# Kernel tuning notes

Measured on AMD Instinct MI355X. Metric: run time of the kernel, lower is better.

Reference implementation:

```python
import jax, jax.numpy as jnp
import numpy as np

NUM_HEADS = 16


def setup_inputs() -> dict:
    key = jax.random.key(0)
    k1, k2, k3 = jax.random.split(key, 3)
    B, N, C = 4, 2048, 1024
    x = jax.random.normal(k1, (B, N, C), dtype=jnp.float32)
    w_qkv = jax.random.normal(k2, (C, 3 * C), dtype=jnp.float32) * (C ** -0.5)
    w_proj = jax.random.normal(k3, (C, C), dtype=jnp.float32) * (C ** -0.5)
    b_proj = jnp.zeros((C,), dtype=jnp.float32)
    return {"x": x, "w_qkv": w_qkv, "w_proj": w_proj, "b_proj": b_proj}


def reference(x, w_qkv, w_proj, b_proj):
    B, N, C = x.shape
    H = NUM_HEADS
    hd = C // H
    scale = hd ** -0.5
    # qkv projection (no bias), split into q, k, v per head
    qkv = jnp.einsum('bnc,cd->bnd', x, w_qkv)            # [B, N, 3C]
    qkv = qkv.reshape(B, N, 3, H, hd).transpose(0, 3, 2, 1, 4)  # [B, H, 3, N, hd]
    q, k, v = qkv[:, :, 0], qkv[:, :, 1], qkv[:, :, 2]   # each [B, H, N, hd]
    q = q * scale
    attn = jax.nn.softmax(jnp.einsum('bhnd,bhmd->bhnm', q, k), axis=-1)  # [B, H, N, N]
    out = jnp.einsum('bhnm,bhmd->bhnd', attn, v)         # [B, H, N, hd]
    out = out.transpose(0, 2, 1, 3).reshape(B, N, C)
    return jnp.einsum('bnc,cd->bnd', out, w_proj) + b_proj
```

## Files before the change

### kernel.cpp

```cpp
#include <hip/hip_runtime.h>

typedef short s16x8 __attribute__((ext_vector_type(8)));
typedef float f32x4 __attribute__((ext_vector_type(4)));
typedef float f32x16 __attribute__((ext_vector_type(16)));
typedef unsigned u32x4 __attribute__((ext_vector_type(4)));


__device__ __forceinline__ unsigned short bf16bits(float f) {
  unsigned u = __builtin_bit_cast(unsigned, f);
  unsigned rnd = 0x7FFFu + ((u >> 16) & 1u);
  return (unsigned short)((u + rnd) >> 16);
}

__device__ __forceinline__ unsigned pk_bf16(float lo, float hi) {
  unsigned r;
  asm("v_cvt_pk_bf16_f32 %0, %1, %2" : "=v"(r) : "v"(lo), "v"(hi));
  return r;
}

__device__ __forceinline__ void async16(const void* g, void* l) {
  __builtin_amdgcn_global_load_lds((const __attribute__((address_space(1))) void*)g,
                                   (__attribute__((address_space(3))) void*)l, 16, 0, 0);
}

__device__ __forceinline__ f32x4 mfma16(s16x8 a, s16x8 b, f32x4 c) {
  return __builtin_amdgcn_mfma_f32_16x16x32_bf16(a, b, c, 0, 0, 0);
}

__device__ __forceinline__ f32x16 mfma32(s16x8 a, s16x8 b, f32x16 c) {
  return __builtin_amdgcn_mfma_f32_32x32x16_bf16(a, b, c, 0, 0, 0);
}

__device__ __forceinline__ s16x8 lds_frag(const unsigned short* S, int row, int c8, int U) {
  int unit = row * U + (c8 ^ (row & (U - 1)));
  return *(const s16x8*)(S + unit * 8);
}


__global__ __launch_bounds__(256) void cvt_f32_bf16(const float4* __restrict__ in,
                                                    unsigned short* __restrict__ out, int n4) {
  int i = blockIdx.x * blockDim.x + threadIdx.x;
  int stride = gridDim.x * blockDim.x;
  for (; i < n4; i += stride) {
    float4 v = in[i];
    uint2 o;
    o.x = pk_bf16(v.x, v.y);
    o.y = pk_bf16(v.z, v.w);
    *(uint2*)(out + (size_t)i * 4) = o;
  }
}

__global__ __launch_bounds__(256) void transpose_f32_bf16(const float* __restrict__ in,
                                                          unsigned short* __restrict__ out,
                                                          int R, int C) {
  __shared__ float tile[32][33];
  int c0 = blockIdx.x * 32, r0 = blockIdx.y * 32;
  int tx = threadIdx.x, ty = threadIdx.y;
  #pragma unroll
  for (int i = 0; i < 32; i += 8)
    tile[ty + i][tx] = in[(size_t)(r0 + ty + i) * C + c0 + tx];
  __syncthreads();
  #pragma unroll
  for (int i = 0; i < 32; i += 8)
    out[(size_t)(c0 + ty + i) * R + r0 + tx] = bf16bits(tile[tx][ty + i]);
}

__global__ __launch_bounds__(256) void transpose_v(const unsigned short* __restrict__ V,
                                                   unsigned short* __restrict__ Vt) {
  __shared__ unsigned short sm[64 * 68];
  int bh = blockIdx.y, kt0 = blockIdx.x * 64;
  const unsigned short* v = V + (size_t)bh * 2048 * 64 + (size_t)kt0 * 64;
  unsigned short* vt = Vt + (size_t)bh * 64 * 2048;
  int t = threadIdx.x;
  #pragma unroll
  for (int i = 0; i < 4; ++i) {
    int u = i * 256 + t;
    int f = u * 4;
    int k = f >> 6, d0 = f & 63;
    *(uint2*)&sm[k * 68 + d0] = *(const uint2*)&v[f];
  }
  __syncthreads();
  #pragma unroll
  for (int j = 0; j < 16; ++j) {
    int o = j * 256 + t;
    int d = o >> 6, k = o & 63;
    vt[(size_t)d * 2048 + kt0 + k] = sm[k * 68 + d];
  }
}


template <typename EPI>
__global__ __launch_bounds__(512, 2) void gemm8(const unsigned short* __restrict__ A,
                                                const unsigned short* __restrict__ Bt,
                                                int K, EPI epi) {
  __shared__ __align__(16) unsigned short As[3 * 128 * 64];
  __shared__ __align__(16) unsigned short Bs[3 * 256 * 64];
  const int tid = threadIdx.x, wid = tid >> 6, lane = tid & 63;
  const int quad = lane >> 4, l16 = lane & 15;
  const int bm0 = blockIdx.y * 128, bn0 = blockIdx.x * 256;
  const int wm = (wid & 1) * 64, wn = (wid >> 1) * 64;
  const int NT = K >> 6;
  f32x4 acc[4][4] = {};

  const int srow = tid >> 3;
  const int sc8 = (tid & 7) ^ (srow & 7);
  auto stage = [&](int s, int tk, int k) {
    int col = tk * 64 + sc8 * 8;
    if (k < 2)
      async16(A + (size_t)(bm0 + k * 64 + srow) * K + col,
              (char*)As + s * 16384 + k * 8192 + wid * 1024);
    else
      async16(Bt + (size_t)(bn0 + (k - 2) * 64 + srow) * K + col,
              (char*)Bs + s * 32768 + (k - 2) * 8192 + wid * 1024);
  };

  #pragma unroll
  for (int k = 0; k < 6; ++k) stage(0, 0, k);
  #pragma unroll
  for (int k = 0; k < 6; ++k) stage(1, 1, k);
  asm volatile("s_waitcnt vmcnt(6)" ::: "memory");
  __builtin_amdgcn_s_barrier();
  __builtin_amdgcn_sched_barrier(0);

  int sc = 0;
  for (int t = 0; t < NT; ++t) {
    const unsigned short* as = As + sc * 8192;
    const unsigned short* bs = Bs + sc * 16384;
    const int sp = (sc == 0) ? 2 : sc - 1;
    const bool pf = (t + 2 < NT);

    #pragma unroll
    for (int kk = 0; kk < 2; ++kk) {
      s16x8 a[4], b[4];
      #pragma unroll
      for (int i = 0; i < 4; ++i) a[i] = lds_frag(as, wm + i * 16 + l16, kk * 4 + quad, 8);
      #pragma unroll
      for (int j = 0; j < 4; ++j) b[j] = lds_frag(bs, wn + j * 16 + l16, kk * 4 + quad, 8);
      if (pf) { stage(sp, t + 2, kk * 3 + 0); stage(sp, t + 2, kk * 3 + 1); stage(sp, t + 2, kk * 3 + 2); }
      __builtin_amdgcn_sched_barrier(0);
      __builtin_amdgcn_s_barrier();
      __builtin_amdgcn_s_setprio(1);
      #pragma unroll
      for (int i = 0; i < 4; ++i)
        #pragma unroll
        for (int j = 0; j < 4; ++j)
          acc[i][j] = mfma16(a[i], b[j], acc[i][j]);
      __builtin_amdgcn_s_setprio(0);
      __builtin_amdgcn_sched_barrier(0);
      if (kk == 1) {
        if (pf) asm volatile("s_waitcnt vmcnt(6)" ::: "memory");
        else    asm volatile("s_waitcnt vmcnt(0)" ::: "memory");
      }
      __builtin_amdgcn_s_barrier();
    }
    sc = (sc == 2) ? 0 : sc + 1;
  }

  #pragma unroll
  for (int i = 0; i < 4; ++i)
    #pragma unroll
    for (int j = 0; j < 4; ++j)
      epi.store4(bm0 + wm + i * 16 + quad * 4, bn0 + wn + j * 16 + l16, acc[i][j]);
}

struct QKVEpi {
  unsigned short *Q, *K, *V;
  float qscale;
  __device__ __forceinline__ void store4(int m0, int n, f32x4 v) const {
    int s = m0 >> 10, h = (m0 >> 6) & 15, d = m0 & 63;
    int b = n >> 11, ns = n & 2047;
    unsigned short* dst = (s == 0) ? Q : ((s == 1) ? K : V);
    float sc = (s == 0) ? qscale : 1.f;
    uint2 o;
    o.x = pk_bf16(v[0] * sc, v[1] * sc);
    o.y = pk_bf16(v[2] * sc, v[3] * sc);
    *(uint2*)&dst[(((size_t)b * 16 + h) * 2048 + ns) * 64 + d] = o;
  }
};

struct ProjEpi {
  const float* bias;
  float* out;
  __device__ __forceinline__ void store4(int m0, int n, f32x4 v) const {
    float4 b4 = *(const float4*)&bias[m0];
    float4 o = {v[0] + b4.x, v[1] + b4.y, v[2] + b4.z, v[3] + b4.w};
    *(float4*)&out[(size_t)n * 1024 + m0] = o;
  }
};

__global__ __launch_bounds__(256, 4) void flash_attn(const unsigned short* __restrict__ Q,
                                                     const unsigned short* __restrict__ K,
                                                     const unsigned short* __restrict__ Vt,
                                                     unsigned short* __restrict__ O) {
  __shared__ __align__(16) unsigned short Ks[2][8 * 512];
  __shared__ __align__(16) unsigned short Vs[2][8 * 512];
  const int tid = threadIdx.x, wid = tid >> 6, lane = tid & 63;
  const int l31 = lane & 31, half = lane >> 5;
  const int bid = blockIdx.y * gridDim.x + blockIdx.x;
  const int xcd = bid & 7, idx = bid >> 3;
  const int bh = xcd * 8 + (idx & 7);
  const int qt = idx >> 3;
  const unsigned short* Qg = Q + (size_t)bh * 2048 * 64;
  const unsigned short* Kg = K + (size_t)bh * 2048 * 64;
  const unsigned short* Vg = Vt + (size_t)bh * 64 * 2048;
  const int qrow = qt * 128 + wid * 32 + l31;

  s16x8 qB[4];
  #pragma unroll
  for (int s = 0; s < 4; ++s)
    qB[s] = *(const s16x8*)&Qg[(size_t)qrow * 64 + s * 16 + half * 8];

  const bool isK = wid < 2;
  int sA[4];
  #pragma unroll
  for (int t = 0; t < 4; ++t) {
    int c = (wid & 1) * 4 + t;
    if (isK) sA[t] = ((c >> 2) * 32 + l31) * 64 + ((c & 3) * 2 + half) * 8;
    else     sA[t] = ((c & 1) * 32 + l31) * 2048 + (c >> 1) * 16 + half * 8;
  }

  auto stage = [&](int kt, int buf) {
    const int kb = kt * 64;
    #pragma unroll
    for (int t = 0; t < 4; ++t) {
      int c = (wid & 1) * 4 + t;
      if (isK) async16(Kg + (size_t)kb * 64 + sA[t], (char*)&Ks[buf][0] + c * 1024);
      else     async16(Vg + kb + sA[t],              (char*)&Vs[buf][0] + c * 1024);
    }
  };

  f32x16 oacc[2] = {};
  float l_i = 0.f;
  const f32x16 fz = {};

  stage(0, 0);
  for (int kt = 0; kt < 32; ++kt) {
    const int cur = kt & 1;
    __syncthreads();
    if (kt + 1 < 32) stage(kt + 1, cur ^ 1);
    const unsigned short* ks = &Ks[cur][0];
    const unsigned short* vs = &Vs[cur][0];

    #pragma unroll
    for (int kf = 0; kf < 2; ++kf) {
      f32x16 st;
      __builtin_amdgcn_s_setprio(1);
      {
        s16x8 a = *(const s16x8*)&ks[((kf * 4 + 0) * 64 + lane) * 8];
        st = mfma32(a, qB[0], fz);
      }
      #pragma unroll
      for (int s = 1; s < 4; ++s) {
        s16x8 a = *(const s16x8*)&ks[((kf * 4 + s) * 64 + lane) * 8];
        st = mfma32(a, qB[s], st);
      }
      __builtin_amdgcn_s_setprio(0);
      float a0 = 0.f, a1 = 0.f, a2 = 0.f, a3 = 0.f;
      #pragma unroll
      for (int r = 0; r < 16; r += 4) {
        float p0 = __builtin_amdgcn_exp2f(st[r + 0]);
        float p1 = __builtin_amdgcn_exp2f(st[r + 1]);
        float p2 = __builtin_amdgcn_exp2f(st[r + 2]);
        float p3 = __builtin_amdgcn_exp2f(st[r + 3]);
        st[r + 0] = p0; st[r + 1] = p1; st[r + 2] = p2; st[r + 3] = p3;
        a0 += p0; a1 += p1; a2 += p2; a3 += p3;
      }
      float rs = (a0 + a1) + (a2 + a3);
      rs += __shfl_xor(rs, 32);
      l_i += rs;
      #pragma unroll
      for (int t = 0; t < 2; ++t) {
        int rb = t * 8;
        unsigned pa0 = pk_bf16(st[rb + 0], st[rb + 1]);
        unsigned pa1 = pk_bf16(st[rb + 2], st[rb + 3]);
        unsigned pb0 = pk_bf16(st[rb + 4], st[rb + 5]);
        unsigned pb1 = pk_bf16(st[rb + 6], st[rb + 7]);
        unsigned s0 = half ? pa0 : pb0;
        unsigned s1 = half ? pa1 : pb1;
        unsigned r0 = (unsigned)__shfl_xor((int)s0, 32);
        unsigned r1 = (unsigned)__shfl_xor((int)s1, 32);
        u32x4 bP;
        bP[0] = half ? r0 : pa0;
        bP[1] = half ? r1 : pa1;
        bP[2] = half ? pb0 : r0;
        bP[3] = half ? pb1 : r1;
        __builtin_amdgcn_s_setprio(1);
        #pragma unroll
        for (int f = 0; f < 2; ++f) {
          s16x8 aV = *(const s16x8*)&vs[(((kf * 2 + t) * 2 + f) * 64 + lane) * 8];
          oacc[f] = mfma32(aV, __builtin_bit_cast(s16x8, bP), oacc[f]);
        }
        __builtin_amdgcn_s_setprio(0);
      }
    }
  }

  const int b = bh >> 4, h = bh & 15;
  float inv = 1.f / l_i;
  size_t base = (((size_t)b * 2048 + qrow) * 16 + h) * 64;
  #pragma unroll
  for (int f = 0; f < 2; ++f)
    #pragma unroll
    for (int q = 0; q < 4; ++q) {
      int d0 = f * 32 + q * 8 + half * 4;
      uint2 o;
      o.x = pk_bf16(oacc[f][q * 4 + 0] * inv, oacc[f][q * 4 + 1] * inv);
      o.y = pk_bf16(oacc[f][q * 4 + 2] * inv, oacc[f][q * 4 + 3] * inv);
      *(uint2*)&O[base + d0] = o;
    }
}


extern "C" void kernel_launch(void* const* d_in, const int* in_sizes, int n_in,
                              void* d_out, int out_size, void* d_ws, size_t ws_size,
                              hipStream_t stream) {
  (void)in_sizes; (void)n_in; (void)out_size; (void)ws_size;
  const float* x = (const float*)d_in[0];
  const float* w_qkv = (const float*)d_in[1];
  const float* w_proj = (const float*)d_in[2];
  const float* b_proj = (const float*)d_in[3];
  float* out = (float*)d_out;
  char* ws = (char*)d_ws;
  const size_t MB = 1ull << 20;
  unsigned short* Xb  = (unsigned short*)(ws);
  unsigned short* Wqt = (unsigned short*)(ws + 16 * MB);
  unsigned short* Wpt = (unsigned short*)(ws + 22 * MB);
  unsigned short* Qb  = (unsigned short*)(ws + 24 * MB);
  unsigned short* Kb  = (unsigned short*)(ws + 40 * MB);
  unsigned short* Vb  = (unsigned short*)(ws + 56 * MB);
  unsigned short* Vt  = Xb;
  unsigned short* Ob  = Vb;

  cvt_f32_bf16<<<2048, 256, 0, stream>>>((const float4*)x, Xb, 8388608 / 4);
  transpose_f32_bf16<<<dim3(96, 32), dim3(32, 8), 0, stream>>>(w_qkv, Wqt, 1024, 3072);
  transpose_f32_bf16<<<dim3(32, 32), dim3(32, 8), 0, stream>>>(w_proj, Wpt, 1024, 1024);

  QKVEpi e1{Qb, Kb, Vb, 0.125f * 1.44269504088896340736f};
  gemm8<QKVEpi><<<dim3(32, 24), 512, 0, stream>>>(Wqt, Xb, 1024, e1);

  transpose_v<<<dim3(32, 64), 256, 0, stream>>>(Vb, Vt);
  flash_attn<<<dim3(16, 64), 256, 0, stream>>>(Qb, Kb, Vt, Ob);

  ProjEpi e2{b_proj, out};
  gemm8<ProjEpi><<<dim3(32, 8), 512, 0, stream>>>(Wpt, Ob, 1024, e2);
}
```

Measured before the change: 276.7 us.

## Enlarge GEMM tile to 256x256 with double-buffered LDS pipeline

Replaces the 128x256 GEMM tile, which used a triple-buffered LDS prefetch two steps ahead, with a 256x256 tile that is double-buffered and prefetches one step ahead. Each wave now computes a 128x64 sub-tile in four phases that reuse the loaded B fragments. The aim is more arithmetic per byte loaded and less global traffic. In exchange it doubles accumulator registers, halves the grid (384 and 128 blocks on a 256-CU part), and leaves less prefetch slack, which risks lower occupancy and poorer wave balance, especially for the projection GEMM.

```diff
diff --git a/kernel.cpp b/kernel.cpp
--- a/kernel.cpp
+++ b/kernel.cpp
@@ -90,74 +90,82 @@
 
 
 template <typename EPI>
-__global__ __launch_bounds__(512, 2) void gemm8(const unsigned short* __restrict__ A,
-                                                const unsigned short* __restrict__ Bt,
-                                                int K, EPI epi) {
-  __shared__ __align__(16) unsigned short As[3 * 128 * 64];
-  __shared__ __align__(16) unsigned short Bs[3 * 256 * 64];
+__global__ __launch_bounds__(512, 2) void gemm256(const unsigned short* __restrict__ A,
+                                                  const unsigned short* __restrict__ Bt,
+                                                  int K, EPI epi) {
+  __shared__ __align__(16) unsigned short As[2 * 256 * 64];
+  __shared__ __align__(16) unsigned short Bs[2 * 256 * 64];
   const int tid = threadIdx.x, wid = tid >> 6, lane = tid & 63;
   const int quad = lane >> 4, l16 = lane & 15;
-  const int bm0 = blockIdx.y * 128, bn0 = blockIdx.x * 256;
-  const int wm = (wid & 1) * 64, wn = (wid >> 1) * 64;
+  const int bm0 = blockIdx.y * 256, bn0 = blockIdx.x * 256;
+  const int wm = (wid & 1) * 128, wn = (wid >> 1) * 64;
   const int NT = K >> 6;
-  f32x4 acc[4][4] = {};
+  f32x4 acc[8][4] = {};
 
   const int srow = tid >> 3;
   const int sc8 = (tid & 7) ^ (srow & 7);
-  auto stage = [&](int s, int tk, int k) {
+  auto stage = [&](int s, int tk, int c) {
     int col = tk * 64 + sc8 * 8;
-    if (k < 2)
-      async16(A + (size_t)(bm0 + k * 64 + srow) * K + col,
-              (char*)As + s * 16384 + k * 8192 + wid * 1024);
+    if (c < 4)
+      async16(A + (size_t)(bm0 + c * 64 + srow) * K + col,
+              (char*)As + s * 32768 + c * 8192 + wid * 1024);
     else
-      async16(Bt + (size_t)(bn0 + (k - 2) * 64 + srow) * K + col,
-              (char*)Bs + s * 32768 + (k - 2) * 8192 + wid * 1024);
+      async16(Bt + (size_t)(bn0 + (c - 4) * 64 + srow) * K + col,
+              (char*)Bs + s * 32768 + (c - 4) * 8192 + wid * 1024);
   };
 
   #pragma unroll
-  for (int k = 0; k < 6; ++k) stage(0, 0, k);
-  #pragma unroll
-  for (int k = 0; k < 6; ++k) stage(1, 1, k);
-  asm volatile("s_waitcnt vmcnt(6)" ::: "memory");
+  for (int c = 0; c < 8; ++c) stage(0, 0, c);
+  asm volatile("s_waitcnt vmcnt(0)" ::: "memory");
   __builtin_amdgcn_s_barrier();
   __builtin_amdgcn_sched_barrier(0);
 
-  int sc = 0;
   for (int t = 0; t < NT; ++t) {
-    const unsigned short* as = As + sc * 8192;
-    const unsigned short* bs = Bs + sc * 16384;
-    const int sp = (sc == 0) ? 2 : sc - 1;
-    const bool pf = (t + 2 < NT);
-
-    #pragma unroll
-    for (int kk = 0; kk < 2; ++kk) {
-      s16x8 a[4], b[4];
-      #pragma unroll
-      for (int i = 0; i < 4; ++i) a[i] = lds_frag(as, wm + i * 16 + l16, kk * 4 + quad, 8);
-      #pragma unroll
-      for (int j = 0; j < 4; ++j) b[j] = lds_frag(bs, wn + j * 16 + l16, kk * 4 + quad, 8);
-      if (pf) { stage(sp, t + 2, kk * 3 + 0); stage(sp, t + 2, kk * 3 + 1); stage(sp, t + 2, kk * 3 + 2); }
+    const int s = t & 1;
+    const unsigned short* as = As + s * 16384;
+    const unsigned short* bs = Bs + s * 16384;
+    const bool pf = (t + 1 < NT);
+    s16x8 b[4][2];
+    #pragma unroll
+    for (int p = 0; p < 4; ++p) {
+      if (p == 0) {
+        #pragma unroll
+        for (int j = 0; j < 4; ++j)
+          #pragma unroll
+          for (int kk = 0; kk < 2; ++kk)
+            b[j][kk] = lds_frag(bs, wn + j * 16 + l16, kk * 4 + quad, 8);
+      }
+      s16x8 a[2][2];
+      #pragma unroll
+      for (int i = 0; i < 2; ++i)
+        #pragma unroll
+        for (int kk = 0; kk < 2; ++kk)
+          a[i][kk] = lds_frag(as, wm + p * 32 + i * 16 + l16, kk * 4 + quad, 8);
+      if (pf && p < 2) {
+        #pragma unroll
+        for (int c = 0; c < 4; ++c) stage(s ^ 1, t + 1, p * 4 + c);
+      }
       __builtin_amdgcn_sched_barrier(0);
       __builtin_amdgcn_s_barrier();
       __builtin_amdgcn_s_setprio(1);
       #pragma unroll
-      for (int i = 0; i < 4; ++i)
-        #pragma unroll
-        for (int j = 0; j < 4; ++j)
-          acc[i][j] = mfma16(a[i], b[j], acc[i][j]);
+      for (int kk = 0; kk < 2; ++kk)
+        #pragma unroll
+        for (int i = 0; i < 2; ++i)
+          #pragma unroll
+          for (int j = 0; j < 4; ++j)
+            acc[p * 2 + i][j] = mfma16(a[i][kk], b[j][kk], acc[p * 2 + i][j]);
       __builtin_amdgcn_s_setprio(0);
       __builtin_amdgcn_sched_barrier(0);
-      if (kk == 1) {
-        if (pf) asm volatile("s_waitcnt vmcnt(6)" ::: "memory");
-        else    asm volatile("s_waitcnt vmcnt(0)" ::: "memory");
-      }
+      if (p == 3)
+        asm volatile("s_waitcnt vmcnt(0)" ::: "memory");
       __builtin_amdgcn_s_barrier();
+      __builtin_amdgcn_sched_barrier(0);
     }
-    sc = (sc == 2) ? 0 : sc + 1;
-  }
-
-  #pragma unroll
-  for (int i = 0; i < 4; ++i)
+  }
+
+  #pragma unroll
+  for (int i = 0; i < 8; ++i)
     #pragma unroll
     for (int j = 0; j < 4; ++j)
       epi.store4(bm0 + wm + i * 16 + quad * 4, bn0 + wn + j * 16 + l16, acc[i][j]);
@@ -336,11 +344,11 @@
   transpose_f32_bf16<<<dim3(32, 32), dim3(32, 8), 0, stream>>>(w_proj, Wpt, 1024, 1024);
 
   QKVEpi e1{Qb, Kb, Vb, 0.125f * 1.44269504088896340736f};
-  gemm8<QKVEpi><<<dim3(32, 24), 512, 0, stream>>>(Wqt, Xb, 1024, e1);
+  gemm256<QKVEpi><<<dim3(32, 12), 512, 0, stream>>>(Wqt, Xb, 1024, e1);
 
   transpose_v<<<dim3(32, 64), 256, 0, stream>>>(Vb, Vt);
   flash_attn<<<dim3(16, 64), 256, 0, stream>>>(Qb, Kb, Vt, Ob);
 
   ProjEpi e2{b_proj, out};
-  gemm8<ProjEpi><<<dim3(32, 8), 512, 0, stream>>>(Wpt, Ob, 1024, e2);
-}
+  gemm256<ProjEpi><<<dim3(32, 4), 512, 0, stream>>>(Wpt, Ob, 1024, e2);
+}
```

After: 297.6 us. +7.5%, slower.

## Switch GEMM to double-buffered LDS with XCD-aware workgroup remapping

Applied to the files above, without the earlier changes.

Changes the GEMM mainloop from a three-stage LDS pipeline with prefetch distance two to a double-buffered pipeline that issues all six async loads for the next tile in the first half-iteration and waits with vmcnt(0) at the end. It also remaps block IDs so that consecutive blocks, which are round-robined across XCDs, share tiles and get better L2 locality. Using less LDS may allow more occupancy, but the shorter prefetch distance and the full wait at the end of each iteration risk exposing memory latency. The remap hardcodes 32 blocks in x.

```diff
diff --git a/kernel.cpp b/kernel.cpp
--- a/kernel.cpp
+++ b/kernel.cpp
@@ -93,11 +93,14 @@
 __global__ __launch_bounds__(512, 2) void gemm8(const unsigned short* __restrict__ A,
                                                 const unsigned short* __restrict__ Bt,
                                                 int K, EPI epi) {
-  __shared__ __align__(16) unsigned short As[3 * 128 * 64];
-  __shared__ __align__(16) unsigned short Bs[3 * 256 * 64];
+  __shared__ __align__(16) unsigned short As[2 * 128 * 64];
+  __shared__ __align__(16) unsigned short Bs[2 * 256 * 64];
   const int tid = threadIdx.x, wid = tid >> 6, lane = tid & 63;
   const int quad = lane >> 4, l16 = lane & 15;
-  const int bm0 = blockIdx.y * 128, bn0 = blockIdx.x * 256;
+  const int bid = blockIdx.y * 32 + blockIdx.x;
+  const int nwg = 32 * gridDim.y;
+  const int wg = (bid & 7) * (nwg >> 3) + (bid >> 3);
+  const int bm0 = (wg >> 5) * 128, bn0 = (wg & 31) * 256;
   const int wm = (wid & 1) * 64, wn = (wid >> 1) * 64;
   const int NT = K >> 6;
   f32x4 acc[4][4] = {};
@@ -116,27 +119,26 @@
 
   #pragma unroll
   for (int k = 0; k < 6; ++k) stage(0, 0, k);
-  #pragma unroll
-  for (int k = 0; k < 6; ++k) stage(1, 1, k);
-  asm volatile("s_waitcnt vmcnt(6)" ::: "memory");
+  asm volatile("s_waitcnt vmcnt(0)" ::: "memory");
   __builtin_amdgcn_s_barrier();
   __builtin_amdgcn_sched_barrier(0);
 
-  int sc = 0;
   for (int t = 0; t < NT; ++t) {
-    const unsigned short* as = As + sc * 8192;
-    const unsigned short* bs = Bs + sc * 16384;
-    const int sp = (sc == 0) ? 2 : sc - 1;
-    const bool pf = (t + 2 < NT);
-
-    #pragma unroll
-    for (int kk = 0; kk < 2; ++kk) {
+    const int s = t & 1;
+    const unsigned short* as = As + s * 8192;
+    const unsigned short* bs = Bs + s * 16384;
+    const bool pf = (t + 1 < NT);
+
+    {
       s16x8 a[4], b[4];
       #pragma unroll
-      for (int i = 0; i < 4; ++i) a[i] = lds_frag(as, wm + i * 16 + l16, kk * 4 + quad, 8);
-      #pragma unroll
-      for (int j = 0; j < 4; ++j) b[j] = lds_frag(bs, wn + j * 16 + l16, kk * 4 + quad, 8);
-      if (pf) { stage(sp, t + 2, kk * 3 + 0); stage(sp, t + 2, kk * 3 + 1); stage(sp, t + 2, kk * 3 + 2); }
+      for (int i = 0; i < 4; ++i) a[i] = lds_frag(as, wm + i * 16 + l16, quad, 8);
+      #pragma unroll
+      for (int j = 0; j < 4; ++j) b[j] = lds_frag(bs, wn + j * 16 + l16, quad, 8);
+      if (pf) {
+        #pragma unroll
+        for (int k = 0; k < 6; ++k) stage(s ^ 1, t + 1, k);
+      }
       __builtin_amdgcn_sched_barrier(0);
       __builtin_amdgcn_s_barrier();
       __builtin_amdgcn_s_setprio(1);
@@ -147,13 +149,29 @@
           acc[i][j] = mfma16(a[i], b[j], acc[i][j]);
       __builtin_amdgcn_s_setprio(0);
       __builtin_amdgcn_sched_barrier(0);
-      if (kk == 1) {
-        if (pf) asm volatile("s_waitcnt vmcnt(6)" ::: "memory");
-        else    asm volatile("s_waitcnt vmcnt(0)" ::: "memory");
-      }
       __builtin_amdgcn_s_barrier();
     }
-    sc = (sc == 2) ? 0 : sc + 1;
+
+    {
+      s16x8 a[4], b[4];
+      #pragma unroll
+      for (int i = 0; i < 4; ++i) a[i] = lds_frag(as, wm + i * 16 + l16, 4 + quad, 8);
+      #pragma unroll
+      for (int j = 0; j < 4; ++j) b[j] = lds_frag(bs, wn + j * 16 + l16, 4 + quad, 8);
+      __builtin_amdgcn_sched_barrier(0);
+      __builtin_amdgcn_s_barrier();
+      __builtin_amdgcn_s_setprio(1);
+      #pragma unroll
+      for (int i = 0; i < 4; ++i)
+        #pragma unroll
+        for (int j = 0; j < 4; ++j)
+          acc[i][j] = mfma16(a[i], b[j], acc[i][j]);
+      __builtin_amdgcn_s_setprio(0);
+      __builtin_amdgcn_sched_barrier(0);
+      asm volatile("s_waitcnt vmcnt(0)" ::: "memory");
+      __builtin_amdgcn_s_barrier();
+      __builtin_amdgcn_sched_barrier(0);
+    }
   }
 
   #pragma unroll
```

Measured after the change: 307.2 us. +11.0%, slower.
